# Optimization experiments

Measured on AMD Instinct MI355X. Metric: run time of the kernel, lower is better.

Reference implementation:

```python
import jax, jax.numpy as jnp
import numpy as np

N = 1572864          # total anchors (P2-P7 pyramid on 1024x1024, 18 anchors/loc)
K = 4096             # fixed NMS candidate budget (jit-compatible top-k prefilter)
IMG_H, IMG_W = 1024, 1024
IOU_THR = 0.1
SCORE_THR = 0.5
BBOX_STD = np.array([0.1, 0.1, 0.2, 0.2], dtype=np.float32)  # RetinaNet BBoxTransform std


def setup_inputs() -> dict:
    key = jax.random.key(0)
    k1, k2, k3, k4 = jax.random.split(key, 4)
    classification = jax.random.uniform(k1, (1, N, 2), dtype=jnp.float32)
    regression = jax.random.normal(k2, (1, N, 4), dtype=jnp.float32)
    ctr = jax.random.uniform(k3, (1, N, 2), dtype=jnp.float32, minval=0.0, maxval=1024.0)
    wh = jax.random.uniform(k4, (1, N, 2), dtype=jnp.float32, minval=16.0, maxval=256.0)
    anchors = jnp.concatenate([ctr - 0.5 * wh, ctr + 0.5 * wh], axis=-1)  # [1,N,4] x1y1x2y2
    return {"classification": classification, "regression": regression,
            "anchors": anchors, "H": IMG_H, "W": IMG_W}


def _decode_clip(anchors, deltas):
    # BBoxTransform: anchors/deltas [1,N,4] -> boxes [N,4], then ClipBoxes to image.
    a = anchors[0]
    d = deltas[0] * jnp.asarray(BBOX_STD)
    w = a[:, 2] - a[:, 0]
    h = a[:, 3] - a[:, 1]
    cx = a[:, 0] + 0.5 * w
    cy = a[:, 1] + 0.5 * h
    pcx = cx + d[:, 0] * w
    pcy = cy + d[:, 1] * h
    pw = jnp.exp(d[:, 2]) * w
    ph = jnp.exp(d[:, 3]) * h
    boxes = jnp.stack([pcx - 0.5 * pw, pcy - 0.5 * ph,
                       pcx + 0.5 * pw, pcy + 0.5 * ph], axis=-1)
    lo = jnp.zeros((4,), jnp.float32)
    hi = jnp.asarray([IMG_W, IMG_H, IMG_W, IMG_H], jnp.float32)
    return jnp.clip(boxes, lo, hi)


def _iou_matrix(b):
    # b: [K,4] -> [K,K] pairwise IoU
    area = (b[:, 2] - b[:, 0]) * (b[:, 3] - b[:, 1])
    lt = jnp.maximum(b[:, None, :2], b[None, :, :2])
    rb = jnp.minimum(b[:, None, 2:], b[None, :, 2:])
    wh = jnp.clip(rb - lt, 0.0)
    inter = wh[..., 0] * wh[..., 1]
    return inter / (area[:, None] + area[None, :] - inter + 1e-8)


def reference(classification, regression, anchors, H, W):
    boxes = _decode_clip(anchors, regression)          # [N,4]
    scores = classification[0, :, 1]                   # [N]
    masked = jnp.where(scores > SCORE_THR, scores, 0.0)
    top_s, order = jax.lax.top_k(masked, K)            # score-sorted candidates
    cand = boxes[order]                                # [K,4]
    iou = _iou_matrix(cand)                            # [K,K]
    valid = top_s > 0.0
    idx = jnp.arange(K)

    def body(keep, i):
        suppress = (iou[i] > IOU_THR) & keep[i] & (idx > i)
        return keep & ~suppress, None

    keep, _ = jax.lax.scan(body, valid, idx)
    keepf = keep.astype(cand.dtype)
    # rescale boxes from model img_shape back to input H,W (factor 1 when H=W=1024)
    scale = jnp.asarray([W / IMG_W, H / IMG_H, W / IMG_W, H / IMG_H], jnp.float32)
    out_boxes = cand * scale * keepf[:, None]
    out_scores = top_s * keepf
    return jnp.concatenate([out_boxes, out_scores[:, None]], axis=-1)  # [K,5]
```

## Files before the change

### kernel.cpp

```cpp
#include <hip/hip_runtime.h>
#include <cstdint>

#define N_TOT 1572864
#define KSEL 4096
#define CAP 8192
#define BINS 4096
#define SCORE_THR 0.5f
#define IOU_THR 0.1f
#define STREAM_BLOCKS 512
#define STAGE 512

__device__ inline uint64_t readlane64(uint64_t v, int lane) {
    uint32_t lo = (uint32_t)__builtin_amdgcn_readlane((int)(uint32_t)v, lane);
    uint32_t hi = (uint32_t)__builtin_amdgcn_readlane((int)(uint32_t)(v >> 32), lane);
    return ((uint64_t)hi << 32) | lo;
}

__global__ void k_init(uint32_t* hist, uint32_t* ctrs, float* topScore) {
    int i = blockIdx.x * blockDim.x + threadIdx.x;
    if (i < BINS) hist[i] = 0;
    if (i < 16) ctrs[i] = 0;
    if (i < KSEL) topScore[i] = 0.0f;
}

__global__ void k_hist(const float4* __restrict__ cls4, uint32_t* __restrict__ hist) {
    int i = blockIdx.x * blockDim.x + threadIdx.x;
    int stride = gridDim.x * blockDim.x;
    for (; i < N_TOT / 2; i += stride) {
        float4 c = cls4[i];
        if (c.y > SCORE_THR) {
            uint32_t bin = (__float_as_uint(c.y) - 0x3F000000u) >> 11;
            if (bin >= BINS) bin = BINS - 1;
            atomicAdd(&hist[bin], 1u);
        }
        if (c.w > SCORE_THR) {
            uint32_t bin = (__float_as_uint(c.w) - 0x3F000000u) >> 11;
            if (bin >= BINS) bin = BINS - 1;
            atomicAdd(&hist[bin], 1u);
        }
    }
}

__global__ void k_thresh(const uint32_t* __restrict__ hist, uint32_t* __restrict__ ctrs) {
    __shared__ uint32_t s_suf[1024];
    int t = threadIdx.x;
    uint32_t l0 = hist[t*4+0], l1 = hist[t*4+1], l2 = hist[t*4+2], l3 = hist[t*4+3];
    s_suf[t] = l0 + l1 + l2 + l3;
    __syncthreads();
    for (int off = 1; off < 1024; off <<= 1) {
        uint32_t v = (t + off < 1024) ? s_suf[t + off] : 0u;
        __syncthreads();
        s_suf[t] += v;
        __syncthreads();
    }
    uint32_t snext = (t < 1023) ? s_suf[t + 1] : 0u;
    uint32_t suf3 = snext + l3;
    uint32_t suf2 = suf3 + l2;
    uint32_t suf1 = suf2 + l1;
    uint32_t suf0 = suf1 + l0;
    uint32_t sufs[5] = {suf0, suf1, suf2, suf3, snext};
    #pragma unroll
    for (int q = 0; q < 4; q++) {
        if (sufs[q] >= KSEL && sufs[q+1] < KSEL) ctrs[1] = (uint32_t)(t*4 + q);
    }
    if (t == 0 && s_suf[0] < KSEL) ctrs[1] = 0;
}

__global__ void k_gather(const float4* __restrict__ cls4, uint32_t* __restrict__ ctrs,
                         uint64_t* __restrict__ keys) {
    __shared__ uint32_t s_cnt;
    __shared__ uint32_t s_base;
    __shared__ uint64_t s_stage[STAGE];
    if (threadIdx.x == 0) s_cnt = 0;
    __syncthreads();

    uint32_t T = ctrs[1];
    uint32_t basebits = 0x3F000000u + (T << 11);
    int i = blockIdx.x * blockDim.x + threadIdx.x;
    int stride = gridDim.x * blockDim.x;
    for (; i < N_TOT / 2; i += stride) {
        float4 c = cls4[i];
        #pragma unroll
        for (int h = 0; h < 2; h++) {
            float s = h ? c.w : c.y;
            uint32_t idx = 2u * (uint32_t)i + (uint32_t)h;
            if (s > SCORE_THR) {
                uint32_t b = __float_as_uint(s);
                if (b >= basebits) {
                    uint64_t key = ((uint64_t)b << 32) | (uint32_t)(~idx);
                    uint32_t p = atomicAdd(&s_cnt, 1u);
                    if (p < STAGE) s_stage[p] = key;
                    else {
                        uint32_t g = atomicAdd(&ctrs[0], 1u);
                        if (g < CAP) keys[g] = key;
                    }
                }
            }
        }
    }
    __syncthreads();
    uint32_t n = s_cnt < STAGE ? s_cnt : STAGE;
    if (threadIdx.x == 0 && n > 0) s_base = atomicAdd(&ctrs[0], n);
    __syncthreads();
    for (uint32_t q = threadIdx.x; q < n; q += blockDim.x) {
        uint32_t g = s_base + q;
        if (g < CAP) keys[g] = s_stage[q];
    }
}

__global__ void k_rankdec(const uint64_t* __restrict__ keys, const uint32_t* __restrict__ ctrs,
                          const float* __restrict__ anchors, const float* __restrict__ reg,
                          float* __restrict__ topScore, float* __restrict__ boxes,
                          float* __restrict__ areas) {
    __shared__ uint64_t s_keys[256];
    uint32_t M = ctrs[0]; if (M > CAP) M = CAP;
    int j = blockIdx.x * blockDim.x + threadIdx.x;
    uint64_t myKey = (j < (int)M) ? keys[j] : 0ull;
    uint32_t rank = 0;
    for (uint32_t base = 0; base < M; base += 256) {
        uint32_t idx = base + threadIdx.x;
        s_keys[threadIdx.x] = (idx < M) ? keys[idx] : 0ull;
        __syncthreads();
        uint32_t lim = min(256u, M - base);
        for (uint32_t q = 0; q < lim; q++)
            rank += (s_keys[q] > myKey) ? 1u : 0u;
        __syncthreads();
    }
    if (j < (int)M && rank < KSEL) {
        uint32_t srcIdx = ~((uint32_t)(myKey & 0xFFFFFFFFull));
        topScore[rank] = __uint_as_float((uint32_t)(myKey >> 32));
        float4 a = *reinterpret_cast<const float4*>(&anchors[(size_t)srcIdx * 4]);
        float4 dd = *reinterpret_cast<const float4*>(&reg[(size_t)srcIdx * 4]);
        float d0 = __fmul_rn(dd.x, 0.1f);
        float d1 = __fmul_rn(dd.y, 0.1f);
        float d2 = __fmul_rn(dd.z, 0.2f);
        float d3 = __fmul_rn(dd.w, 0.2f);
        float w  = __fsub_rn(a.z, a.x);
        float h  = __fsub_rn(a.w, a.y);
        float cx = __fadd_rn(a.x, __fmul_rn(0.5f, w));
        float cy = __fadd_rn(a.y, __fmul_rn(0.5f, h));
        float pcx = __fadd_rn(cx, __fmul_rn(d0, w));
        float pcy = __fadd_rn(cy, __fmul_rn(d1, h));
        float pw = __fmul_rn((float)exp((double)d2), w);
        float ph = __fmul_rn((float)exp((double)d3), h);
        float x0 = __fsub_rn(pcx, __fmul_rn(0.5f, pw));
        float y0 = __fsub_rn(pcy, __fmul_rn(0.5f, ph));
        float x1 = __fadd_rn(pcx, __fmul_rn(0.5f, pw));
        float y1 = __fadd_rn(pcy, __fmul_rn(0.5f, ph));
        x0 = fminf(fmaxf(x0, 0.0f), 1024.0f);
        y0 = fminf(fmaxf(y0, 0.0f), 1024.0f);
        x1 = fminf(fmaxf(x1, 0.0f), 1024.0f);
        y1 = fminf(fmaxf(y1, 0.0f), 1024.0f);
        *reinterpret_cast<float4*>(&boxes[(size_t)rank * 4]) = make_float4(x0, y0, x1, y1);
        areas[rank] = __fmul_rn(__fsub_rn(x1, x0), __fsub_rn(y1, y0));
    }
}

__global__ void k_mask(const float* __restrict__ boxes, const float* __restrict__ areas,
                       unsigned long long* __restrict__ rowmask) {
    int bi = blockIdx.y, bj = blockIdx.x;
    int t = threadIdx.x;
    if (bj < bi) {
        rowmask[(size_t)(bi * 64 + t) * 64 + bj] = 0ull;
        return;
    }
    __shared__ float s_box[64][4];
    __shared__ float s_area[64];
    int r0 = bi * 64 + t;
    s_box[t][0] = boxes[r0 * 4 + 0];
    s_box[t][1] = boxes[r0 * 4 + 1];
    s_box[t][2] = boxes[r0 * 4 + 2];
    s_box[t][3] = boxes[r0 * 4 + 3];
    s_area[t] = areas[r0];
    __syncthreads();
    int j = bj * 64 + t;
    float jx0 = boxes[j * 4 + 0], jy0 = boxes[j * 4 + 1], jx1 = boxes[j * 4 + 2], jy1 = boxes[j * 4 + 3];
    float ja = areas[j];
    unsigned long long myword = 0ull;
    #pragma unroll 4
    for (int r = 0; r < 64; r++) {
        int i = bi * 64 + r;
        float w = __fsub_rn(fminf(s_box[r][2], jx1), fmaxf(s_box[r][0], jx0));
        float h = __fsub_rn(fminf(s_box[r][3], jy1), fmaxf(s_box[r][1], jy0));
        w = fmaxf(w, 0.0f); h = fmaxf(h, 0.0f);
        float inter = __fmul_rn(w, h);
        float denom = __fadd_rn(__fsub_rn(__fadd_rn(s_area[r], ja), inter), 1e-8f);
        float iou = __fdiv_rn(inter, denom);
        bool sup = (iou > IOU_THR) && (j > i);
        unsigned long long b = __ballot(sup);
        if (t == r) myword = b;
    }
    rowmask[(size_t)(bi * 64 + t) * 64 + bj] = myword;
}

__global__ void k_reduce(const float* __restrict__ topScore,
                         const unsigned long long* __restrict__ rowmask,
                         const float* __restrict__ boxes,
                         const int* __restrict__ Hp, const int* __restrict__ Wp,
                         float* __restrict__ out) {
    int w = threadIdx.x;
    uint64_t keep = 0ull;
    #pragma unroll
    for (int c = 0; c < 64; c += 4) {
        float4 s4 = *reinterpret_cast<const float4*>(&topScore[w * 64 + c]);
        keep |= ((uint64_t)(s4.x > 0.0f) << (c + 0))
             |  ((uint64_t)(s4.y > 0.0f) << (c + 1))
             |  ((uint64_t)(s4.z > 0.0f) << (c + 2))
             |  ((uint64_t)(s4.w > 0.0f) << (c + 3));
    }

    uint64_t dg0 = rowmask[(size_t)(0 * 64 + w) * 64 + 0];
    uint64_t dg1 = rowmask[(size_t)(1 * 64 + w) * 64 + 1];

    for (int b = 0; b < 64; b++) {
        uint64_t diag = dg0;
        dg0 = dg1;
        int nb = (b + 2 < 64) ? (b + 2) : 63;
        dg1 = rowmask[(size_t)(nb * 64 + w) * 64 + nb];

        uint32_t klo = (uint32_t)__builtin_amdgcn_readlane((int)(uint32_t)keep, b);
        uint32_t khi = (uint32_t)__builtin_amdgcn_readlane((int)(uint32_t)(keep >> 32), b);
        uint64_t kw = ((uint64_t)khi << 32) | klo;
        uint64_t rem = kw;
        while (rem) {
            int i = __builtin_ctzll(rem);
            rem &= rem - 1;
            uint64_t row = readlane64(diag, i);
            kw &= ~row;
            rem &= ~row;
        }

        uint64_t acc = 0ull;
        uint64_t rem2 = kw;
        const unsigned long long* base = rowmask + (size_t)(b * 64) * 64 + w;
        while (rem2) {
            int i0 = __builtin_ctzll(rem2); uint64_t r = rem2 & (rem2 - 1);
            int i1 = r ? __builtin_ctzll(r) : i0; r = r ? (r & (r - 1)) : r;
            int i2 = r ? __builtin_ctzll(r) : i0; r = r ? (r & (r - 1)) : r;
            int i3 = r ? __builtin_ctzll(r) : i0; r = r ? (r & (r - 1)) : r;
            int i4 = r ? __builtin_ctzll(r) : i0; r = r ? (r & (r - 1)) : r;
            int i5 = r ? __builtin_ctzll(r) : i0; r = r ? (r & (r - 1)) : r;
            int i6 = r ? __builtin_ctzll(r) : i0; r = r ? (r & (r - 1)) : r;
            int i7 = r ? __builtin_ctzll(r) : i0; r = r ? (r & (r - 1)) : r;
            rem2 = r;
            uint64_t r0 = base[(size_t)i0 * 64];
            uint64_t r1 = base[(size_t)i1 * 64];
            uint64_t r2 = base[(size_t)i2 * 64];
            uint64_t r3 = base[(size_t)i3 * 64];
            uint64_t r4 = base[(size_t)i4 * 64];
            uint64_t r5 = base[(size_t)i5 * 64];
            uint64_t r6 = base[(size_t)i6 * 64];
            uint64_t r7 = base[(size_t)i7 * 64];
            acc |= (r0 | r1) | (r2 | r3) | ((r4 | r5) | (r6 | r7));
        }
        keep &= ~acc;
    }

    float sx = (float)((double)Wp[0] / 1024.0);
    float sy = (float)((double)Hp[0] / 1024.0);
    for (int c = 0; c < 64; c++) {
        int k = w * 64 + c;
        float f = ((keep >> c) & 1ull) ? 1.0f : 0.0f;
        float4 bx = *reinterpret_cast<const float4*>(&boxes[(size_t)k * 4]);
        out[k * 5 + 0] = __fmul_rn(__fmul_rn(bx.x, sx), f);
        out[k * 5 + 1] = __fmul_rn(__fmul_rn(bx.y, sy), f);
        out[k * 5 + 2] = __fmul_rn(__fmul_rn(bx.z, sx), f);
        out[k * 5 + 3] = __fmul_rn(__fmul_rn(bx.w, sy), f);
        out[k * 5 + 4] = __fmul_rn(topScore[k], f);
    }
}

extern "C" void kernel_launch(void* const* d_in, const int* in_sizes, int n_in,
                              void* d_out, int out_size, void* d_ws, size_t ws_size,
                              hipStream_t stream) {
    (void)in_sizes; (void)n_in; (void)out_size; (void)ws_size;
    const float4* cls4   = (const float4*)d_in[0];
    const float* reg     = (const float*)d_in[1];
    const float* anchors = (const float*)d_in[2];
    const int* Hp        = (const int*)d_in[3];
    const int* Wp        = (const int*)d_in[4];
    float* out = (float*)d_out;

    char* ws = (char*)d_ws;
    size_t off = 0;
    auto alloc = [&](size_t bytes) {
        char* p = ws + off;
        off = (off + bytes + 255) & ~(size_t)255;
        return p;
    };
    uint32_t* hist   = (uint32_t*)alloc(BINS * 4);
    uint32_t* ctrs   = (uint32_t*)alloc(64);
    uint64_t* keys   = (uint64_t*)alloc((size_t)CAP * 8);
    float* topScore  = (float*)alloc(KSEL * 4);
    float* boxes     = (float*)alloc(KSEL * 4 * 4);
    float* areas     = (float*)alloc(KSEL * 4);
    unsigned long long* rowmask = (unsigned long long*)alloc((size_t)KSEL * 64 * 8);

    k_init<<<16, 256, 0, stream>>>(hist, ctrs, topScore);
    k_hist<<<STREAM_BLOCKS, 256, 0, stream>>>(cls4, hist);
    k_thresh<<<1, 1024, 0, stream>>>(hist, ctrs);
    k_gather<<<STREAM_BLOCKS, 256, 0, stream>>>(cls4, ctrs, keys);
    k_rankdec<<<CAP / 256, 256, 0, stream>>>(keys, ctrs, anchors, reg, topScore, boxes, areas);
    dim3 mg(64, 64);
    k_mask<<<mg, 64, 0, stream>>>(boxes, areas, rowmask);
    k_reduce<<<1, 64, 0, stream>>>(topScore, rowmask, boxes, Hp, Wp, out);
}
```

Before: 231.8 us.

## Prefetch full rowmask block rows in reduce loop and mask-OR instead of sparse gathers

The serial NMS reduce loop now loads all 64 rows of each rowmask block unconditionally, split into two halves held in register buffers. The first half of the next block is issued before the current block's reduction finishes, so its loads overlap the diagonal-resolution work. The data-dependent sparse gather loop on kept bits is replaced with a branchless masked OR. This trades more memory traffic and about 128 extra VGPRs for hiding load latency on the single-wave critical path.

```diff
diff --git a/kernel.cpp b/kernel.cpp
--- a/kernel.cpp
+++ b/kernel.cpp
@@ -193,6 +193,23 @@
     rowmask[(size_t)(bi * 64 + t) * 64 + bj] = myword;
 }
 
+__device__ __forceinline__ void issue_rows(const unsigned long long* __restrict__ rowmask,
+                                           int b, int half, int w, uint64_t (&buf)[32]) {
+    const unsigned long long* p = rowmask + (size_t)(b * 64 + half * 32) * 64 + w;
+    #pragma unroll
+    for (int i = 0; i < 32; i++) buf[i] = p[(size_t)i * 64];
+}
+
+__device__ __forceinline__ uint64_t or_rows(uint64_t kwhalf, const uint64_t (&buf)[32]) {
+    uint64_t acc = 0ull;
+    #pragma unroll
+    for (int i = 0; i < 32; i++) {
+        uint64_t m = (uint64_t)0 - ((kwhalf >> i) & 1ull);
+        acc |= buf[i] & m;
+    }
+    return acc;
+}
+
 __global__ void k_reduce(const float* __restrict__ topScore,
                          const unsigned long long* __restrict__ rowmask,
                          const float* __restrict__ boxes,
@@ -209,10 +226,13 @@
              |  ((uint64_t)(s4.w > 0.0f) << (c + 3));
     }
 
+    uint64_t A[32], B[32];
+    issue_rows(rowmask, 0, 0, w, A);
     uint64_t dg0 = rowmask[(size_t)(0 * 64 + w) * 64 + 0];
     uint64_t dg1 = rowmask[(size_t)(1 * 64 + w) * 64 + 1];
 
     for (int b = 0; b < 64; b++) {
+        issue_rows(rowmask, b, 1, w, B);
         uint64_t diag = dg0;
         dg0 = dg1;
         int nb = (b + 2 < 64) ? (b + 2) : 63;
@@ -230,29 +250,9 @@
             rem &= ~row;
         }
 
-        uint64_t acc = 0ull;
-        uint64_t rem2 = kw;
-        const unsigned long long* base = rowmask + (size_t)(b * 64) * 64 + w;
-        while (rem2) {
-            int i0 = __builtin_ctzll(rem2); uint64_t r = rem2 & (rem2 - 1);
-            int i1 = r ? __builtin_ctzll(r) : i0; r = r ? (r & (r - 1)) : r;
-            int i2 = r ? __builtin_ctzll(r) : i0; r = r ? (r & (r - 1)) : r;
-            int i3 = r ? __builtin_ctzll(r) : i0; r = r ? (r & (r - 1)) : r;
-            int i4 = r ? __builtin_ctzll(r) : i0; r = r ? (r & (r - 1)) : r;
-            int i5 = r ? __builtin_ctzll(r) : i0; r = r ? (r & (r - 1)) : r;
-            int i6 = r ? __builtin_ctzll(r) : i0; r = r ? (r & (r - 1)) : r;
-            int i7 = r ? __builtin_ctzll(r) : i0; r = r ? (r & (r - 1)) : r;
-            rem2 = r;
-            uint64_t r0 = base[(size_t)i0 * 64];
-            uint64_t r1 = base[(size_t)i1 * 64];
-            uint64_t r2 = base[(size_t)i2 * 64];
-            uint64_t r3 = base[(size_t)i3 * 64];
-            uint64_t r4 = base[(size_t)i4 * 64];
-            uint64_t r5 = base[(size_t)i5 * 64];
-            uint64_t r6 = base[(size_t)i6 * 64];
-            uint64_t r7 = base[(size_t)i7 * 64];
-            acc |= (r0 | r1) | (r2 | r3) | ((r4 | r5) | (r6 | r7));
-        }
+        uint64_t acc = or_rows(kw, A);
+        if (b + 1 < 64) issue_rows(rowmask, b + 1, 0, w, A);
+        acc |= or_rows(kw >> 32, B);
         keep &= ~acc;
     }
 
```

Measured after the change: 834.2 us. 3.6x slower.
